# Kernel optimization log

Measured on AMD Instinct MI355X. Metric: run time of the kernel, lower is better.

The kernel has to match this reference:

```python
import jax, jax.numpy as jnp
import numpy as np

T, B = 256, 256
OBS, FEAT, A = 512, 512, 15
H = FEAT + A + 1  # lstm_output_size = feature_dim + num_actions + 1 = 528


def setup_inputs() -> dict:
    key = jax.random.key(0)
    ks = jax.random.split(key, 16)
    s = 0.05
    f32 = jnp.float32
    return {
        "obs": jax.random.normal(ks[0], (T, B, OBS), f32),
        "last_action": jax.random.randint(ks[1], (T, B), 0, A, dtype=jnp.int32),
        "reward": jax.random.normal(ks[2], (T, B), f32),
        "terminated": jax.random.bernoulli(ks[3], 0.05, (T, B)),
        # encoder Linear(OBS -> FEAT)
        "W_enc": jax.random.normal(ks[4], (FEAT, OBS), f32) * s,
        "b_enc": jnp.zeros((FEAT,), f32),
        # 2-layer LSTM, input size == hidden size == H, torch gate order i,f,g,o
        "w_ih0": jax.random.normal(ks[5], (4 * H, H), f32) * s,
        "w_hh0": jax.random.normal(ks[6], (4 * H, H), f32) * s,
        "b_ih0": jnp.zeros((4 * H,), f32),
        "b_hh0": jnp.zeros((4 * H,), f32),
        "w_ih1": jax.random.normal(ks[7], (4 * H, H), f32) * s,
        "w_hh1": jax.random.normal(ks[8], (4 * H, H), f32) * s,
        "b_ih1": jnp.zeros((4 * H,), f32),
        "b_hh1": jnp.zeros((4 * H,), f32),
        # heads
        "W_pol": jax.random.normal(ks[9], (A, H), f32) * s,
        "b_pol": jnp.zeros((A,), f32),
        "W_base": jax.random.normal(ks[10], (1, H), f32) * s,
        "b_base": jnp.zeros((1,), f32),
    }


def reference(obs, last_action, reward, terminated,
              W_enc, b_enc,
              w_ih0, w_hh0, b_ih0, b_hh0,
              w_ih1, w_hh1, b_ih1, b_hh1,
              W_pol, b_pol, W_base, b_base):
    Tn, Bn = obs.shape[0], obs.shape[1]
    feats = jax.nn.relu(jnp.einsum('tbo,fo->tbf', obs, W_enc) + b_enc)
    one_hot = jax.nn.one_hot(last_action, A, dtype=feats.dtype)
    clipped_r = jnp.clip(reward, -1.0, 1.0)[..., None]
    x = jnp.concatenate([feats, clipped_r, one_hot], axis=-1)  # [T,B,H]
    nd = (~terminated).astype(x.dtype)[..., None]              # [T,B,1]

    w_ih = (w_ih0, w_ih1)
    w_hh = (w_hh0, w_hh1)
    b_ih = (b_ih0, b_ih1)
    b_hh = (b_hh0, b_hh1)

    def step(carry, inp):
        h, c = carry          # each [2,B,H]
        x_t, nd_t = inp       # [B,H], [B,1]
        h = h * nd_t          # done-mask reset of state, per original loop
        c = c * nd_t
        inp_l = x_t
        new_h, new_c = [], []
        for l in range(2):
            gates = inp_l @ w_ih[l].T + b_ih[l] + h[l] @ w_hh[l].T + b_hh[l]
            i, f, g, o = jnp.split(gates, 4, axis=-1)
            c_l = jax.nn.sigmoid(f) * c[l] + jax.nn.sigmoid(i) * jnp.tanh(g)
            h_l = jax.nn.sigmoid(o) * jnp.tanh(c_l)
            new_h.append(h_l)
            new_c.append(c_l)
            inp_l = h_l
        return (jnp.stack(new_h), jnp.stack(new_c)), inp_l

    h0 = jnp.zeros((2, Bn, H), x.dtype)  # init_state: zeros
    c0 = jnp.zeros((2, Bn, H), x.dtype)
    (hT, cT), lstm_out = jax.lax.scan(step, (h0, c0), (x, nd))  # lstm_out [T,B,H]

    policy_logits = lstm_out @ W_pol.T + b_pol          # [T,B,A]
    baseline = (lstm_out @ W_base.T + b_base)[..., 0]   # [T,B]
    action = jax.random.categorical(jax.random.key(1), policy_logits, axis=-1)  # [T,B]
    return policy_logits, baseline, action, hT, cT
```

## Files before the change

kernel.cpp:

```cpp
#include <hip/hip_runtime.h>
#include <stdint.h>
#include <math.h>

#define TSTEPS 256
#define BATCH  256
#define OBS_D  512
#define FEATD  512
#define NACT   15
#define HDIM   528
#define HB     (HDIM*BATCH)

#define OFF_ND    0
#define OFF_FLAG  65536
#define ALW_BYTES 262208
#define SB        91952
#define FXT       (SB)
#define FH0       (FXT + 4*HB)
#define FH1       (FH0 + 2*HB)
#define FC0       (FH1 + 2*HB)
#define FC1       (FC0 + HB)
#define FST_END   (FC1 + HB)

#define DBS0   0
#define DBS1   2112
#define DBENC  4224
#define DHW    4736
#define DHB    13184
#define DALW_N 13200

#define OUT_POL   0
#define OUT_BASE  983040
#define OUT_ACT   1048576
#define OUT_H     1114112
#define OUT_C     1384448

__device__ __forceinline__ float sigf_(float x){ return 1.0f/(1.0f+expf(-x)); }

__device__ __forceinline__ uint32_t rotl32_(uint32_t x, uint32_t d){
  return (x<<d)|(x>>(32u-d));
}

__device__ double gumbel_for(uint32_t idx){
  uint32_t x0 = 0u, x1 = idx;
  const uint32_t k0 = 0u, k1 = 1u;
  const uint32_t ks[3] = {k0, k1, 0x1BD11BDAu ^ k0 ^ k1};
  x0 += ks[0]; x1 += ks[1];
  const uint32_t R0[4] = {13u,15u,26u,6u}, R1[4] = {17u,29u,16u,24u};
  #pragma unroll
  for (int g=0; g<5; ++g){
    const uint32_t* r = (g&1) ? R1 : R0;
    #pragma unroll
    for (int j=0;j<4;++j){ x0 += x1; x1 = rotl32_(x1, r[j]); x1 ^= x0; }
    x0 += ks[(g+1)%3];
    x1 += ks[(g+2)%3] + (uint32_t)(g+1);
  }
  const uint32_t bits = x0 ^ x1;
  float u = __uint_as_float((bits>>9) | 0x3f800000u) - 1.0f;
  const float TINY = 1.17549435e-38f;
  u = u * (1.0f - TINY) + TINY;
  u = fmaxf(TINY, u);
  return -log(-log((double)u));
}

__global__ void zero_kernel(float* __restrict__ p, int n){
  int i = blockIdx.x*256 + threadIdx.x;
  if (i < n) p[i] = 0.0f;
}

__global__ void detect_term_kernel(const void* __restrict__ term, int* __restrict__ flag){
  __shared__ int s_nf, s_nb, s_ni;
  if (threadIdx.x==0){ s_nf=0; s_nb=0; s_ni=0; }
  __syncthreads();
  const uint8_t*  pb = (const uint8_t*)term;
  const uint32_t* pw = (const uint32_t*)term;
  int nf=0, nb=0, ni=0;
  for (int i=threadIdx.x; i<16384; i+=256){
    uint32_t v = pw[i];
    if (v == 0x3F800000u) nf++;
    if (v == 1u) ni++;
  }
  for (int o=threadIdx.x; o<65536; o+=256){
    if ((o&3) && pb[o]) nb++;
  }
  if (nf) atomicAdd(&s_nf, nf);
  if (nb) atomicAdd(&s_nb, nb);
  if (ni) atomicAdd(&s_ni, ni);
  __syncthreads();
  if (threadIdx.x==0){
    flag[0] = (s_nf>0) ? 2 : ((s_nb>0) ? 0 : ((s_ni>0) ? 1 : 0));
  }
}

__global__ void nd_kernel(const void* __restrict__ term, const int* __restrict__ flag,
                          float* __restrict__ nd){
  int i = blockIdx.x*256 + threadIdx.x;
  if (i >= TSTEPS*BATCH) return;
  int f = flag[0];
  bool done;
  if (f == 0)      done = ((const uint8_t*)term)[i] != 0;
  else if (f == 1) done = ((const int*)term)[i] != 0;
  else             done = ((const float*)term)[i] != 0.0f;
  nd[i] = done ? 0.0f : 1.0f;
}

__global__ void prep_small_kernel(float* __restrict__ alw,
    const float* __restrict__ bih0, const float* __restrict__ bhh0,
    const float* __restrict__ bih1, const float* __restrict__ bhh1,
    const float* __restrict__ benc,
    const float* __restrict__ Wpol, const float* __restrict__ bpol,
    const float* __restrict__ Wbase, const float* __restrict__ bbase){
  int i = blockIdx.x*256 + threadIdx.x;
  if (i >= DALW_N) return;
  if (i < 2112)            alw[DBS0 + i] = bih0[i] + bhh0[i];
  else if (i < 4224)       { int j=i-2112; alw[DBS1 + j] = bih1[j] + bhh1[j]; }
  else if (i < 4736)       { int j=i-4224; alw[DBENC + j] = benc[j]; }
  else if (i < 13184)      { int j=i-4736; int r=j/HDIM, k=j%HDIM;
                             alw[DHW + j] = (r<NACT ? Wpol[r*HDIM+k] : Wbase[k]); }
  else                     { int j=i-13184; alw[DHB + j] = (j<NACT ? bpol[j] : bbase[0]); }
}

__device__ __forceinline__ void lstm_block(
    int jt, int step, const float* __restrict__ srcA, const float* __restrict__ srcB,
    const float* __restrict__ wih, const float* __restrict__ whh,
    const float* __restrict__ bsum,
    const float* __restrict__ nd, float* __restrict__ cbuf, float* __restrict__ hout,
    int b)
{
  const int j0 = jt*2;
  const float ndv = nd[step*BATCH + b];
  float acc[8];
  const float* wA[8]; const float* wB[8];
  #pragma unroll
  for (int c=0;c<8;++c){
    const int col = (c>>1)*HDIM + j0 + (c&1);
    acc[c] = bsum[col];
    wA[c] = wih + (size_t)col*HDIM;
    wB[c] = whh + (size_t)col*HDIM;
  }
  const float* a = srcA + b;
  #pragma unroll 8
  for (int k=0;k<HDIM;++k){
    const float xv = a[(size_t)k*BATCH];
    #pragma unroll
    for (int c=0;c<8;++c) acc[c] = fmaf(wA[c][k], xv, acc[c]);
  }
  const float* bb = srcB + b;
  #pragma unroll 8
  for (int k=0;k<HDIM;++k){
    const float hv = bb[(size_t)k*BATCH] * ndv;
    #pragma unroll
    for (int c=0;c<8;++c) acc[c] = fmaf(wB[c][k], hv, acc[c]);
  }
  #pragma unroll
  for (int jj=0;jj<2;++jj){
    const float gi=acc[0+jj], gf=acc[2+jj], gg=acc[4+jj], go=acc[6+jj];
    const int idx=(j0+jj)*BATCH+b;
    const float cold = cbuf[idx]*ndv;
    const float cn = sigf_(gf)*cold + sigf_(gi)*tanhf(gg);
    const float hn = sigf_(go)*tanhf(cn);
    cbuf[idx]=cn; hout[idx]=hn;
  }
}

__global__ __launch_bounds__(256) void step_kernel(
  const float* __restrict__ obs, const int* __restrict__ lastAct,
  const float* __restrict__ reward,
  const float* __restrict__ wenc,
  const float* __restrict__ wih0, const float* __restrict__ whh0,
  const float* __restrict__ wih1, const float* __restrict__ whh1,
  float* __restrict__ ws, float* __restrict__ alw,
  float* __restrict__ out, int t)
{
  const int bid = blockIdx.x;
  const int b = threadIdx.x;
  float* nd = ws + OFF_ND;
  float* xT = ws + FXT;
  float* h0 = ws + FH0;
  float* h1 = ws + FH1;
  float* c0 = ws + FC0;
  float* c1 = ws + FC1;

  if (bid < 264) {
    if (t < 0 || t > 255) return;
    lstm_block(bid, t,
               xT + (size_t)(t&3)*HB,
               h0 + (size_t)((t+1)&1)*HB,
               wih0, whh0, alw + DBS0, nd, c0,
               h0 + (size_t)(t&1)*HB, b);
  } else if (bid < 528) {
    const int s = t - 1;
    if (s < 0 || s > 255) return;
    lstm_block(bid-264, s,
               h0 + (size_t)(s&1)*HB,
               h1 + (size_t)((s+1)&1)*HB,
               wih1, whh1, alw + DBS1, nd, c1,
               h1 + (size_t)(s&1)*HB, b);
  } else if (bid < 593) {
    const int te = t + 2;
    if (te < 0 || te > 255) return;
    float* xs = xT + (size_t)(te&3)*HB;
    if (bid < 592) {
      const int e = bid - 528;
      const int f0 = e*8;
      float acc[8];
      const float* wrow[8];
      #pragma unroll
      for (int c=0;c<8;++c){ acc[c]=alw[DBENC+f0+c]; wrow[c]=wenc+(size_t)(f0+c)*OBS_D; }
      __shared__ float lx[32][257];
      const int r0 = threadIdx.x>>3;
      const int kk = (threadIdx.x&7)<<2;
      for (int kc=0; kc<OBS_D; kc+=32){
        __syncthreads();
        #pragma unroll
        for (int rr=0; rr<256; rr+=32){
          const float4 v = *(const float4*)(obs + ((size_t)te*BATCH + (r0+rr))*OBS_D + kc + kk);
          lx[kk+0][r0+rr]=v.x; lx[kk+1][r0+rr]=v.y; lx[kk+2][r0+rr]=v.z; lx[kk+3][r0+rr]=v.w;
        }
        __syncthreads();
        #pragma unroll 4
        for (int k2=0;k2<32;++k2){
          const float xv = lx[k2][b];
          #pragma unroll
          for (int c=0;c<8;++c) acc[c] = fmaf(xv, wrow[c][kc+k2], acc[c]);
        }
      }
      #pragma unroll
      for (int c=0;c<8;++c) xs[(size_t)(f0+c)*BATCH + b] = fmaxf(acc[c], 0.0f);
    } else {
      const float r = reward[te*BATCH + b];
      xs[(size_t)FEATD*BATCH + b] = fminf(fmaxf(r, -1.0f), 1.0f);
      const int la = lastAct[te*BATCH + b];
      #pragma unroll
      for (int a2=0; a2<NACT; ++a2)
        xs[(size_t)(FEATD+1+a2)*BATCH + b] = (a2==la) ? 1.0f : 0.0f;
    }
  } else {
    const int s = t - 2;
    if (s < 0 || s > 255) return;
    const float* hsrc = h1 + (size_t)(s&1)*HB;
    float acc[16];
    #pragma unroll
    for (int c=0;c<16;++c) acc[c]=alw[DHB+c];
    const float* hb = hsrc + b;
    #pragma unroll 4
    for (int k=0;k<HDIM;++k){
      const float hv = hb[(size_t)k*BATCH];
      #pragma unroll
      for (int c=0;c<16;++c) acc[c] = fmaf(hv, alw[DHW + (size_t)c*HDIM + k], acc[c]);
    }
    const int row = s*BATCH + b;
    #pragma unroll
    for (int c=0;c<15;++c) out[OUT_POL + (size_t)row*NACT + c] = acc[c];
    out[OUT_BASE + row] = acc[15];
    double best = -1.0e300; int bi = 0;
    #pragma unroll
    for (int a2=0; a2<NACT; ++a2){
      const double v = (double)acc[a2] + gumbel_for((uint32_t)(row*NACT + a2));
      if (v > best){ best = v; bi = a2; }
    }
    out[OUT_ACT + row] = (float)bi;
  }
}

__global__ void finalize_kernel(const float* __restrict__ ws, float* __restrict__ out){
  int i = blockIdx.x*256 + threadIdx.x;
  if (i >= 2*HB) return;
  const int l = i / HB;
  const int r = i % HB;
  const int bq = r / HDIM;
  const int j  = r % HDIM;
  const float* hf = ws + (l==0 ? FH0 : FH1) + HB;
  const float* cf = ws + (l==0 ? FC0 : FC1);
  out[OUT_H + i] = hf[(size_t)j*BATCH + bq];
  out[OUT_C + i] = cf[(size_t)j*BATCH + bq];
}

extern "C" void kernel_launch(void* const* d_in, const int* in_sizes, int n_in,
                              void* d_out, int out_size, void* d_ws, size_t ws_size,
                              hipStream_t stream) {
  const float* obs     = (const float*)d_in[0];
  const int*   lastAct = (const int*)  d_in[1];
  const float* reward  = (const float*)d_in[2];
  const void*  term    =               d_in[3];
  const float* Wenc    = (const float*)d_in[4];
  const float* benc    = (const float*)d_in[5];
  const float* wih0    = (const float*)d_in[6];
  const float* whh0    = (const float*)d_in[7];
  const float* bih0    = (const float*)d_in[8];
  const float* bhh0    = (const float*)d_in[9];
  const float* wih1    = (const float*)d_in[10];
  const float* whh1    = (const float*)d_in[11];
  const float* bih1    = (const float*)d_in[12];
  const float* bhh1    = (const float*)d_in[13];
  const float* Wpol    = (const float*)d_in[14];
  const float* bpol    = (const float*)d_in[15];
  const float* Wbase   = (const float*)d_in[16];
  const float* bbase   = (const float*)d_in[17];
  float*  ws   = (float*)d_ws;
  int*    flag = (int*)(ws + OFF_FLAG);
  float*  alw  = (float*)((char*)d_ws + ALW_BYTES);
  float*  out  = (float*)d_out;

  {
    const int nz = 6*HB;
    zero_kernel<<<(nz+255)/256, 256, 0, stream>>>(ws + FH0, nz);
  }
  detect_term_kernel<<<1, 256, 0, stream>>>(term, flag);
  nd_kernel<<<(TSTEPS*BATCH+255)/256, 256, 0, stream>>>(term, flag, ws + OFF_ND);
  prep_small_kernel<<<(DALW_N+255)/256, 256, 0, stream>>>(alw,
      bih0, bhh0, bih1, bhh1, benc, Wpol, bpol, Wbase, bbase);

  for (int t = -2; t <= 257; ++t) {
    step_kernel<<<594, 256, 0, stream>>>(
      obs, lastAct, reward,
      Wenc, wih0, whh0, wih1, whh1,
      ws, alw, out, t);
  }
  finalize_kernel<<<(2*HB+255)/256, 256, 0, stream>>>(ws, out);
}
```

Baseline: 22.29 ms.

## Move LSTM gate GEMMs to bf16x3 split-precision MFMA with packed activations

Replaces the per-thread scalar FMA LSTM gate computation with MFMA 16x16x32 bf16 instructions. Each fp32 operand is split into high and low bf16 parts and three products are summed to keep near-fp32 accuracy. Weights are converted and staged through double-buffered shared memory each step. Activations (x, h0, h1) are stored batch-major as hi/lo bf16 pairs, and the grid shrinks from 594 to 330 blocks. This removes the scalar FMA bottleneck of the recurrent matmuls, at the cost of reconverting weights every step and some precision risk.

```diff
diff --git a/kernel.cpp b/kernel.cpp
--- a/kernel.cpp
+++ b/kernel.cpp
@@ -9,17 +9,23 @@
 #define NACT   15
 #define HDIM   528
 #define HB     (HDIM*BATCH)
-
-#define OFF_ND    0
-#define OFF_FLAG  65536
-#define ALW_BYTES 262208
-#define SB        91952
-#define FXT       (SB)
-#define FH0       (FXT + 4*HB)
-#define FH1       (FH0 + 2*HB)
-#define FC0       (FH1 + 2*HB)
-#define FC1       (FC0 + HB)
-#define FST_END   (FC1 + HB)
+#define PK     544
+
+typedef __attribute__((ext_vector_type(8))) short short8v;
+typedef __attribute__((ext_vector_type(4))) short short4v;
+typedef __attribute__((ext_vector_type(4))) float float4v;
+
+#define OFF_ND_B     0
+#define OFF_FLAG_B   262144
+#define OFF_ALW_B    262208
+#define XP_B         315392
+#define SLOT_B       557056
+#define PL_B         278528
+#define H0P_B        1986560
+#define H1P_B        3100672
+#define C0_B         4214784
+#define C1_B         4755456
+#define WS_END_B     5296128
 
 #define DBS0   0
 #define DBS1   2112
@@ -35,6 +41,15 @@
 #define OUT_C     1384448
 
 __device__ __forceinline__ float sigf_(float x){ return 1.0f/(1.0f+expf(-x)); }
+
+__device__ __forceinline__ unsigned short f2bf(float f){
+  unsigned u = __float_as_uint(f);
+  unsigned r = (u + 0x7FFFu + ((u>>16)&1u)) >> 16;
+  return (unsigned short)r;
+}
+__device__ __forceinline__ float bf2f(unsigned short s){
+  return __uint_as_float(((unsigned)s)<<16);
+}
 
 __device__ __forceinline__ uint32_t rotl32_(uint32_t x, uint32_t d){
   return (x<<d)|(x>>(32u-d));
@@ -119,47 +134,129 @@
   else                     { int j=i-13184; alw[DHB + j] = (j<NACT ? bpol[j] : bbase[0]); }
 }
 
-__device__ __forceinline__ void lstm_block(
-    int jt, int step, const float* __restrict__ srcA, const float* __restrict__ srcB,
+__device__ __forceinline__ void lstm_mfma(
+    unsigned short* __restrict__ smem_u,
+    int j16, int nb, int step,
+    const unsigned short* __restrict__ bAh, const unsigned short* __restrict__ bAl,
+    const unsigned short* __restrict__ bBh, const unsigned short* __restrict__ bBl,
+    unsigned short* __restrict__ oHh, unsigned short* __restrict__ oHl,
     const float* __restrict__ wih, const float* __restrict__ whh,
-    const float* __restrict__ bsum,
-    const float* __restrict__ nd, float* __restrict__ cbuf, float* __restrict__ hout,
-    int b)
+    const float* __restrict__ bsum, const float* __restrict__ nd,
+    float* __restrict__ cbuf, int tid)
 {
-  const int j0 = jt*2;
+  const int w = tid>>6, l = tid&63;
+  const int j0 = j16*16, n0 = nb*64;
+  const int sr = tid&63, kq = tid>>6;
+  const int gate = sr>>4, jr = j0 + (sr&15);
+  const float* rih = wih + (size_t)(gate*528 + jr)*528;
+  const float* rhh = whh + (size_t)(gate*528 + jr)*528;
+  const short8v zv = {0,0,0,0,0,0,0,0};
+
+  bool ndm[4];
+  #pragma unroll
+  for (int s=0;s<4;++s) ndm[s] = nd[step*BATCH + n0 + s*16 + (l&15)] != 0.0f;
+
+  float4v acc[4];
+  #pragma unroll
+  for (int s=0;s<4;++s) acc[s] = (float4v){0.f,0.f,0.f,0.f};
+
+  auto STAGE = [&](int cc, int bsel){
+    const int vk0 = cc*64 + kq*16;
+    float v[16];
+    if (vk0 < 528){
+      const float4* p = (const float4*)(rih + vk0);
+      #pragma unroll
+      for (int q=0;q<4;++q){ float4 x = p[q]; v[q*4]=x.x; v[q*4+1]=x.y; v[q*4+2]=x.z; v[q*4+3]=x.w; }
+    } else if (vk0 < 544){
+      #pragma unroll
+      for (int i=0;i<16;++i) v[i]=0.0f;
+    } else if (vk0 < 1072){
+      const float4* p = (const float4*)(rhh + (vk0-544));
+      #pragma unroll
+      for (int q=0;q<4;++q){ float4 x = p[q]; v[q*4]=x.x; v[q*4+1]=x.y; v[q*4+2]=x.z; v[q*4+3]=x.w; }
+    } else {
+      #pragma unroll
+      for (int i=0;i<16;++i) v[i]=0.0f;
+    }
+    short8v hA, hB, lA, lB;
+    #pragma unroll
+    for (int i=0;i<8;++i){
+      unsigned short hb = f2bf(v[i]);
+      hA[i] = (short)hb; lA[i] = (short)f2bf(v[i] - bf2f(hb));
+    }
+    #pragma unroll
+    for (int i=0;i<8;++i){
+      unsigned short hb = f2bf(v[8+i]);
+      hB[i] = (short)hb; lB[i] = (short)f2bf(v[8+i] - bf2f(hb));
+    }
+    unsigned short* dh = smem_u + bsel*9216 + sr*72 + kq*16;
+    *(short8v*)(dh)          = hA;
+    *(short8v*)(dh + 8)      = hB;
+    *(short8v*)(dh + 4608)   = lA;
+    *(short8v*)(dh + 4616)   = lB;
+  };
+
+  auto KSTEP = [&](int ks){
+    const unsigned short* sl = smem_u + ((ks>>1)&1)*9216;
+    const int aoff = (16*w + (l&15))*72 + (ks&1)*32 + ((l>>4)<<3);
+    const short8v ah = *(const short8v*)(sl + aoff);
+    const short8v al = *(const short8v*)(sl + 4608 + aoff);
+    const bool second = (ks >= 17);
+    const int kin = (second ? (ks-17)*32 : ks*32) + ((l>>4)<<3);
+    const unsigned short* ph  = second ? bBh : bAh;
+    const unsigned short* pl2 = second ? bBl : bAl;
+    #pragma unroll
+    for (int s=0;s<4;++s){
+      const int n = n0 + s*16 + (l&15);
+      short8v bh = *(const short8v*)(ph  + (size_t)n*PK + kin);
+      short8v bl = *(const short8v*)(pl2 + (size_t)n*PK + kin);
+      if (second && !ndm[s]){ bh = zv; bl = zv; }
+      acc[s] = __builtin_amdgcn_mfma_f32_16x16x32_bf16(ah, bh, acc[s], 0,0,0);
+      acc[s] = __builtin_amdgcn_mfma_f32_16x16x32_bf16(ah, bl, acc[s], 0,0,0);
+      acc[s] = __builtin_amdgcn_mfma_f32_16x16x32_bf16(al, bh, acc[s], 0,0,0);
+    }
+  };
+
+  STAGE(0, 0);
+  __syncthreads();
+  #pragma unroll 1
+  for (int cc=0; cc<17; ++cc){
+    if (cc < 16) STAGE(cc+1, (cc+1)&1);
+    KSTEP(2*cc); KSTEP(2*cc+1);
+    __syncthreads();
+  }
+
+  float* gf = (float*)smem_u;
+  #pragma unroll
+  for (int s=0;s<4;++s){
+    #pragma unroll
+    for (int r2=0;r2<4;++r2)
+      gf[w*1088 + (((l>>4)<<2)+r2)*68 + s*16 + (l&15)] = acc[s][r2];
+  }
+  __syncthreads();
+
+  const int bl = tid&63, j4 = tid>>6;
+  const int b = n0 + bl;
   const float ndv = nd[step*BATCH + b];
-  float acc[8];
-  const float* wA[8]; const float* wB[8];
+  short4v hv, lv;
   #pragma unroll
-  for (int c=0;c<8;++c){
-    const int col = (c>>1)*HDIM + j0 + (c&1);
-    acc[c] = bsum[col];
-    wA[c] = wih + (size_t)col*HDIM;
-    wB[c] = whh + (size_t)col*HDIM;
-  }
-  const float* a = srcA + b;
-  #pragma unroll 8
-  for (int k=0;k<HDIM;++k){
-    const float xv = a[(size_t)k*BATCH];
-    #pragma unroll
-    for (int c=0;c<8;++c) acc[c] = fmaf(wA[c][k], xv, acc[c]);
-  }
-  const float* bb = srcB + b;
-  #pragma unroll 8
-  for (int k=0;k<HDIM;++k){
-    const float hv = bb[(size_t)k*BATCH] * ndv;
-    #pragma unroll
-    for (int c=0;c<8;++c) acc[c] = fmaf(wB[c][k], hv, acc[c]);
-  }
-  #pragma unroll
-  for (int jj=0;jj<2;++jj){
-    const float gi=acc[0+jj], gf=acc[2+jj], gg=acc[4+jj], go=acc[6+jj];
-    const int idx=(j0+jj)*BATCH+b;
+  for (int jj=0;jj<4;++jj){
+    const int jloc = j4*4 + jj, j = j0 + jloc;
+    const float gi = gf[0*1088 + jloc*68 + bl] + bsum[j];
+    const float gff= gf[1*1088 + jloc*68 + bl] + bsum[528 + j];
+    const float gg = gf[2*1088 + jloc*68 + bl] + bsum[1056 + j];
+    const float go = gf[3*1088 + jloc*68 + bl] + bsum[1584 + j];
+    const int idx = j*BATCH + b;
     const float cold = cbuf[idx]*ndv;
-    const float cn = sigf_(gf)*cold + sigf_(gi)*tanhf(gg);
+    const float cn = sigf_(gff)*cold + sigf_(gi)*tanhf(gg);
     const float hn = sigf_(go)*tanhf(cn);
-    cbuf[idx]=cn; hout[idx]=hn;
-  }
+    cbuf[idx] = cn;
+    const unsigned short hb = f2bf(hn);
+    hv[jj] = (short)hb;
+    lv[jj] = (short)f2bf(hn - bf2f(hb));
+  }
+  *(short4v*)(oHh + (size_t)b*PK + j0 + j4*4) = hv;
+  *(short4v*)(oHl + (size_t)b*PK + j0 + j4*4) = lv;
 }
 
 __global__ __launch_bounds__(256) void step_kernel(
@@ -171,82 +268,131 @@
   float* __restrict__ ws, float* __restrict__ alw,
   float* __restrict__ out, int t)
 {
+  __shared__ unsigned short smem_u[18432];
   const int bid = blockIdx.x;
-  const int b = threadIdx.x;
-  float* nd = ws + OFF_ND;
-  float* xT = ws + FXT;
-  float* h0 = ws + FH0;
-  float* h1 = ws + FH1;
-  float* c0 = ws + FC0;
-  float* c1 = ws + FC1;
-
-  if (bid < 264) {
-    if (t < 0 || t > 255) return;
-    lstm_block(bid, t,
-               xT + (size_t)(t&3)*HB,
-               h0 + (size_t)((t+1)&1)*HB,
-               wih0, whh0, alw + DBS0, nd, c0,
-               h0 + (size_t)(t&1)*HB, b);
-  } else if (bid < 528) {
-    const int s = t - 1;
-    if (s < 0 || s > 255) return;
-    lstm_block(bid-264, s,
-               h0 + (size_t)(s&1)*HB,
-               h1 + (size_t)((s+1)&1)*HB,
-               wih1, whh1, alw + DBS1, nd, c1,
-               h1 + (size_t)(s&1)*HB, b);
-  } else if (bid < 593) {
+  const int tid = threadIdx.x;
+  float* nd = (float*)((char*)ws + OFF_ND_B);
+  char* wsc = (char*)ws;
+
+  if (bid < 264){
+    const int layer = (bid < 132) ? 0 : 1;
+    const int rr = layer ? bid-132 : bid;
+    const int step = layer ? t-1 : t;
+    if (step < 0 || step > 255) return;
+    const int j16 = rr>>2, nb = rr&3;
+    const unsigned short *bAh,*bAl,*bBh,*bBl; unsigned short *oHh,*oHl;
+    const float *wih,*whh,*bsum; float* cbuf;
+    if (layer == 0){
+      const int sl = step%3, pp = (step+1)&1, po = step&1;
+      bAh = (const unsigned short*)(wsc + XP_B + sl*SLOT_B);
+      bAl = (const unsigned short*)(wsc + XP_B + sl*SLOT_B + PL_B);
+      bBh = (const unsigned short*)(wsc + H0P_B + pp*SLOT_B);
+      bBl = (const unsigned short*)(wsc + H0P_B + pp*SLOT_B + PL_B);
+      oHh = (unsigned short*)(wsc + H0P_B + po*SLOT_B);
+      oHl = (unsigned short*)(wsc + H0P_B + po*SLOT_B + PL_B);
+      wih = wih0; whh = whh0; bsum = alw + DBS0;
+      cbuf = (float*)(wsc + C0_B);
+    } else {
+      const int pa = step&1, pb2 = (step+1)&1;
+      bAh = (const unsigned short*)(wsc + H0P_B + pa*SLOT_B);
+      bAl = (const unsigned short*)(wsc + H0P_B + pa*SLOT_B + PL_B);
+      bBh = (const unsigned short*)(wsc + H1P_B + pb2*SLOT_B);
+      bBl = (const unsigned short*)(wsc + H1P_B + pb2*SLOT_B + PL_B);
+      oHh = (unsigned short*)(wsc + H1P_B + pa*SLOT_B);
+      oHl = (unsigned short*)(wsc + H1P_B + pa*SLOT_B + PL_B);
+      wih = wih1; whh = whh1; bsum = alw + DBS1;
+      cbuf = (float*)(wsc + C1_B);
+    }
+    lstm_mfma(smem_u, j16, nb, step, bAh, bAl, bBh, bBl, oHh, oHl,
+              wih, whh, bsum, nd, cbuf, tid);
+  } else if (bid < 328){
     const int te = t + 2;
     if (te < 0 || te > 255) return;
-    float* xs = xT + (size_t)(te&3)*HB;
-    if (bid < 592) {
-      const int e = bid - 528;
-      const int f0 = e*8;
-      float acc[8];
-      const float* wrow[8];
-      #pragma unroll
-      for (int c=0;c<8;++c){ acc[c]=alw[DBENC+f0+c]; wrow[c]=wenc+(size_t)(f0+c)*OBS_D; }
-      __shared__ float lx[32][257];
-      const int r0 = threadIdx.x>>3;
-      const int kk = (threadIdx.x&7)<<2;
-      for (int kc=0; kc<OBS_D; kc+=32){
-        __syncthreads();
+    const int sl = te%3;
+    unsigned short* xh = (unsigned short*)(wsc + XP_B + sl*SLOT_B);
+    unsigned short* xl = (unsigned short*)(wsc + XP_B + sl*SLOT_B + PL_B);
+    float (*lx)[257] = (float(*)[257])smem_u;
+    const int e = bid - 264;
+    const int f0 = e*8;
+    const int b = tid;
+    float acc[8];
+    const float* wrow[8];
+    #pragma unroll
+    for (int c=0;c<8;++c){ acc[c]=alw[DBENC+f0+c]; wrow[c]=wenc+(size_t)(f0+c)*OBS_D; }
+    const int r0 = tid>>3;
+    const int kk = (tid&7)<<2;
+    for (int kc=0; kc<OBS_D; kc+=32){
+      __syncthreads();
+      #pragma unroll
+      for (int rr2=0; rr2<256; rr2+=32){
+        const float4 v = *(const float4*)(obs + ((size_t)te*BATCH + (r0+rr2))*OBS_D + kc + kk);
+        lx[kk+0][r0+rr2]=v.x; lx[kk+1][r0+rr2]=v.y; lx[kk+2][r0+rr2]=v.z; lx[kk+3][r0+rr2]=v.w;
+      }
+      __syncthreads();
+      #pragma unroll 4
+      for (int k2=0;k2<32;++k2){
+        const float xv = lx[k2][b];
         #pragma unroll
-        for (int rr=0; rr<256; rr+=32){
-          const float4 v = *(const float4*)(obs + ((size_t)te*BATCH + (r0+rr))*OBS_D + kc + kk);
-          lx[kk+0][r0+rr]=v.x; lx[kk+1][r0+rr]=v.y; lx[kk+2][r0+rr]=v.z; lx[kk+3][r0+rr]=v.w;
-        }
-        __syncthreads();
-        #pragma unroll 4
-        for (int k2=0;k2<32;++k2){
-          const float xv = lx[k2][b];
-          #pragma unroll
-          for (int c=0;c<8;++c) acc[c] = fmaf(xv, wrow[c][kc+k2], acc[c]);
-        }
+        for (int c=0;c<8;++c) acc[c] = fmaf(xv, wrow[c][kc+k2], acc[c]);
       }
-      #pragma unroll
-      for (int c=0;c<8;++c) xs[(size_t)(f0+c)*BATCH + b] = fmaxf(acc[c], 0.0f);
-    } else {
-      const float r = reward[te*BATCH + b];
-      xs[(size_t)FEATD*BATCH + b] = fminf(fmaxf(r, -1.0f), 1.0f);
-      const int la = lastAct[te*BATCH + b];
-      #pragma unroll
-      for (int a2=0; a2<NACT; ++a2)
-        xs[(size_t)(FEATD+1+a2)*BATCH + b] = (a2==la) ? 1.0f : 0.0f;
-    }
+    }
+    short8v hv, lv;
+    #pragma unroll
+    for (int c=0;c<8;++c){
+      const float v = fmaxf(acc[c], 0.0f);
+      const unsigned short hb = f2bf(v);
+      hv[c] = (short)hb; lv[c] = (short)f2bf(v - bf2f(hb));
+    }
+    *(short8v*)(xh + (size_t)b*PK + f0) = hv;
+    *(short8v*)(xl + (size_t)b*PK + f0) = lv;
+  } else if (bid == 328){
+    const int te = t + 2;
+    if (te < 0 || te > 255) return;
+    const int sl = te%3;
+    unsigned short* xh = (unsigned short*)(wsc + XP_B + sl*SLOT_B);
+    unsigned short* xl = (unsigned short*)(wsc + XP_B + sl*SLOT_B + PL_B);
+    const int b = tid;
+    float vals[16];
+    const float r = reward[te*BATCH + b];
+    vals[0] = fminf(fmaxf(r, -1.0f), 1.0f);
+    const int la = lastAct[te*BATCH + b];
+    #pragma unroll
+    for (int a2=0; a2<NACT; ++a2) vals[1+a2] = (a2==la) ? 1.0f : 0.0f;
+    short8v hv0, lv0, hv1, lv1;
+    #pragma unroll
+    for (int i=0;i<8;++i){
+      unsigned short hb = f2bf(vals[i]);
+      hv0[i]=(short)hb; lv0[i]=(short)f2bf(vals[i]-bf2f(hb));
+    }
+    #pragma unroll
+    for (int i=0;i<8;++i){
+      unsigned short hb = f2bf(vals[8+i]);
+      hv1[i]=(short)hb; lv1[i]=(short)f2bf(vals[8+i]-bf2f(hb));
+    }
+    *(short8v*)(xh + (size_t)b*PK + 512) = hv0;
+    *(short8v*)(xh + (size_t)b*PK + 520) = hv1;
+    *(short8v*)(xl + (size_t)b*PK + 512) = lv0;
+    *(short8v*)(xl + (size_t)b*PK + 520) = lv1;
   } else {
     const int s = t - 2;
     if (s < 0 || s > 255) return;
-    const float* hsrc = h1 + (size_t)(s&1)*HB;
+    const int pa = s&1;
+    const unsigned short* hh = (const unsigned short*)(wsc + H1P_B + pa*SLOT_B);
+    const unsigned short* hl = (const unsigned short*)(wsc + H1P_B + pa*SLOT_B + PL_B);
+    const int b = tid;
     float acc[16];
     #pragma unroll
     for (int c=0;c<16;++c) acc[c]=alw[DHB+c];
-    const float* hb = hsrc + b;
-    #pragma unroll 4
-    for (int k=0;k<HDIM;++k){
-      const float hv = hb[(size_t)k*BATCH];
-      #pragma unroll
-      for (int c=0;c<16;++c) acc[c] = fmaf(hv, alw[DHW + (size_t)c*HDIM + k], acc[c]);
+    for (int kc=0; kc<66; ++kc){
+      const short8v H = *(const short8v*)(hh + (size_t)b*PK + kc*8);
+      const short8v L = *(const short8v*)(hl + (size_t)b*PK + kc*8);
+      #pragma unroll
+      for (int u=0;u<8;++u){
+        const float hv = bf2f((unsigned short)H[u]) + bf2f((unsigned short)L[u]);
+        const int k = kc*8+u;
+        #pragma unroll
+        for (int c=0;c<16;++c) acc[c] = fmaf(hv, alw[DHW + (size_t)c*HDIM + k], acc[c]);
+      }
     }
     const int row = s*BATCH + b;
     #pragma unroll
@@ -265,13 +411,15 @@
 __global__ void finalize_kernel(const float* __restrict__ ws, float* __restrict__ out){
   int i = blockIdx.x*256 + threadIdx.x;
   if (i >= 2*HB) return;
+  const char* wsc = (const char*)ws;
   const int l = i / HB;
   const int r = i % HB;
   const int bq = r / HDIM;
   const int j  = r % HDIM;
-  const float* hf = ws + (l==0 ? FH0 : FH1) + HB;
-  const float* cf = ws + (l==0 ? FC0 : FC1);
-  out[OUT_H + i] = hf[(size_t)j*BATCH + bq];
+  const unsigned short* hh = (const unsigned short*)(wsc + (l==0?H0P_B:H1P_B) + 1*SLOT_B);
+  const unsigned short* hl = hh + PL_B/2;
+  const float* cf = (const float*)(wsc + (l==0?C0_B:C1_B));
+  out[OUT_H + i] = bf2f(hh[(size_t)bq*PK + j]) + bf2f(hl[(size_t)bq*PK + j]);
   out[OUT_C + i] = cf[(size_t)j*BATCH + bq];
 }
 
@@ -297,21 +445,21 @@
   const float* Wbase   = (const float*)d_in[16];
   const float* bbase   = (const float*)d_in[17];
   float*  ws   = (float*)d_ws;
-  int*    flag = (int*)(ws + OFF_FLAG);
-  float*  alw  = (float*)((char*)d_ws + ALW_BYTES);
+  int*    flag = (int*)((char*)d_ws + OFF_FLAG_B);
+  float*  alw  = (float*)((char*)d_ws + OFF_ALW_B);
   float*  out  = (float*)d_out;
 
   {
-    const int nz = 6*HB;
-    zero_kernel<<<(nz+255)/256, 256, 0, stream>>>(ws + FH0, nz);
+    const int nz = (WS_END_B - XP_B)/4;
+    zero_kernel<<<(nz+255)/256, 256, 0, stream>>>(ws + XP_B/4, nz);
   }
   detect_term_kernel<<<1, 256, 0, stream>>>(term, flag);
-  nd_kernel<<<(TSTEPS*BATCH+255)/256, 256, 0, stream>>>(term, flag, ws + OFF_ND);
+  nd_kernel<<<(TSTEPS*BATCH+255)/256, 256, 0, stream>>>(term, flag, (float*)((char*)d_ws + OFF_ND_B));
   prep_small_kernel<<<(DALW_N+255)/256, 256, 0, stream>>>(alw,
       bih0, bhh0, bih1, bhh1, benc, Wpol, bpol, Wbase, bbase);
 
   for (int t = -2; t <= 257; ++t) {
-    step_kernel<<<594, 256, 0, stream>>>(
+    step_kernel<<<330, 256, 0, stream>>>(
       obs, lastAct, reward,
       Wenc, wih0, whh0, wih1, whh1,
       ws, alw, out, t);
```

After: 26.78 ms. +20.2%, slower.
